# Kernel optimization log

Hardware: AMD Instinct MI355X
Metric: run time of the kernel (lower is better)

Reference implementation:

```python
import jax, jax.numpy as jnp
import numpy as np

B, S, HID = 1, 1024, 4096
NH, NKV, HD = 32, 8, 128
GROUPS = NH // NKV
THETA = 10000.0
SPAR = 0.5          # sparse_aggression (layer_idx > 0)
MIN_IDX = 4         # min_sparse_index: always-kept sink tokens
NEG = jnp.float32(-1e30)


def setup_inputs() -> dict:
    key = jax.random.key(0)
    k0, k1, k2, k3, k4 = jax.random.split(key, 5)
    sc = 0.02
    return {
        "hidden_states": jax.random.normal(k0, (B, S, HID), jnp.float32),
        "position_ids": jnp.arange(S, dtype=jnp.int32)[None, :],
        "Wq": jax.random.normal(k1, (NH * HD, HID), jnp.float32) * sc,
        "Wk": jax.random.normal(k2, (NKV * HD, HID), jnp.float32) * sc,
        "Wv": jax.random.normal(k3, (NKV * HD, HID), jnp.float32) * sc,
        "Wo": jax.random.normal(k4, (HID, NH * HD), jnp.float32) * sc,
    }


def _rotate_half(x):
    h = x.shape[-1] // 2
    return jnp.concatenate([-x[..., h:], x[..., :h]], axis=-1)


def _rope_cos_sin(position_ids):
    inv_freq = 1.0 / (THETA ** (jnp.arange(0, HD, 2, dtype=jnp.float32) / HD))
    freqs = position_ids.astype(jnp.float32)[..., None] * inv_freq  # [B,S,HD/2]
    emb = jnp.concatenate([freqs, freqs], axis=-1)                  # [B,S,HD]
    return jnp.cos(emb)[:, None], jnp.sin(emb)[:, None]             # [B,1,S,HD]


def reference(hidden_states, position_ids, Wq, Wk, Wv, Wo):
    b, s, _ = hidden_states.shape
    # QKV projections (nn.Linear: x @ W.T)
    q = (hidden_states @ Wq.T).reshape(b, s, NH, HD).transpose(0, 2, 1, 3)
    k = (hidden_states @ Wk.T).reshape(b, s, NKV, HD).transpose(0, 2, 1, 3)
    v = (hidden_states @ Wv.T).reshape(b, s, NKV, HD).transpose(0, 2, 1, 3)
    # RoPE
    cos, sin = _rope_cos_sin(position_ids)
    q = q * cos + _rotate_half(q) * sin
    k = k * cos + _rotate_half(k) * sin
    # repeat_kv (GQA expansion)
    k = jnp.repeat(k, GROUPS, axis=1)
    v = jnp.repeat(v, GROUPS, axis=1)
    # causal additive mask [1,1,S,S]
    causal = jnp.where(jnp.triu(jnp.ones((s, s), bool), 1), NEG, jnp.float32(0))[None, None]
    scale = 1.0 / np.sqrt(HD)
    scores = jnp.einsum('bhqd,bhkd->bhqk', q, k) * scale
    # oracle importance: softmax of (softmaxed) masked attention (no_grad in original)
    oracle = jax.nn.softmax((scores + causal).astype(jnp.float32), axis=-1)
    importance = jax.nn.softmax(oracle, axis=-1)
    importance = jax.lax.stop_gradient(importance)
    # descending sort -> rank of each key for each query
    sorted_idx = jnp.argsort(-importance, axis=-1)          # [B,H,S,S]
    ranks = jnp.argsort(sorted_idx, axis=-1)                # inverse perm
    # per-query token budget: keep ceil-ish top-k proportional to row length
    k_per_row = jnp.maximum((SPAR * (jnp.arange(s) + 1)).astype(jnp.int32), 1)
    key_idx = jnp.arange(s)
    kept = (ranks < k_per_row[None, None, :, None]) | (key_idx[None, None, None, :] < MIN_IDX)
    sparse_mask = jnp.where(kept, jnp.float32(0), NEG)
    # sparse attention
    attn = scores + sparse_mask + causal
    probs = jax.nn.softmax(attn.astype(jnp.float32), axis=-1).astype(v.dtype)
    out = jnp.einsum('bhqk,bhkd->bhqd', probs, v)           # [B,H,S,HD]
    out = out.transpose(0, 2, 1, 3).reshape(b, s, NH * HD)
    return out @ Wo.T
```

## Files before the change

kernel.cpp:

```cpp
#include <hip/hip_runtime.h>
#include <hip/hip_bf16.h>

#define S_LEN 1024
#define HID   4096
#define NH    32
#define NKV   8
#define HD    128
#define MIN_IDX 4
#define AO_COLS 4096
#define HEAD_STRIDE 131072

typedef __attribute__((ext_vector_type(8))) short short8;
typedef __attribute__((ext_vector_type(4))) float f32x4;

__device__ __forceinline__ unsigned short f2bf(float f) {
  union { float f; unsigned u; } v; v.f = f;
  unsigned r = v.u + 0x7FFFu + ((v.u >> 16) & 1u);
  return (unsigned short)(r >> 16);
}
__device__ __forceinline__ float bf2f(unsigned short h) {
  union { unsigned u; float f; } v; v.u = ((unsigned)h) << 16;
  return v.f;
}
__device__ __forceinline__ unsigned pk2(float a, float b) {
  union { __hip_bfloat162 h; unsigned u; } c;
  c.h = __float22bfloat162_rn(make_float2(a, b));
  return c.u;
}
__device__ __forceinline__ short8 pack8(float4 a, float4 b) {
  union { short8 s; unsigned u[4]; } r;
  r.u[0] = pk2(a.x, a.y); r.u[1] = pk2(a.z, a.w);
  r.u[2] = pk2(b.x, b.y); r.u[3] = pk2(b.z, b.w);
  return r.s;
}
__device__ __forceinline__ unsigned ordf(float f) {
  union { float f; int i; } v; v.f = f;
  return (unsigned)(v.i ^ ((v.i >> 31) | 0x80000000));
}
__device__ __forceinline__ float iordf(unsigned u) {
  union { int i; float f; } v;
  v.i = (u & 0x80000000u) ? (int)(u ^ 0x80000000u) : (int)~u;
  return v.f;
}
__device__ __forceinline__ float wave_sum_f(float v) {
  #pragma unroll
  for (int m = 32; m >= 1; m >>= 1) v += __shfl_xor(v, m);
  return v;
}
__device__ __forceinline__ unsigned wave_max_u(unsigned v) {
  #pragma unroll
  for (int m = 32; m >= 1; m >>= 1) { unsigned o = __shfl_xor(v, m); v = o > v ? o : v; }
  return v;
}
__device__ __forceinline__ void wave_lds_fence() {
  __builtin_amdgcn_s_waitcnt(0);
  __builtin_amdgcn_wave_barrier();
}
__device__ __forceinline__ void gload_lds16(const unsigned short* g, unsigned short* l) {
  auto gp = (const __attribute__((address_space(1))) unsigned*)g;
  auto lp = (__attribute__((address_space(3))) unsigned*)(unsigned)(unsigned long long)l;
  __builtin_amdgcn_global_load_lds(gp, lp, 16, 0, 0);
}

__global__ __launch_bounds__(256) void cvt_k(
    const float* __restrict__ src, unsigned short* __restrict__ dst)
{
  const size_t i = ((size_t)blockIdx.x * 256 + threadIdx.x) * 8;
  float4 a = *(const float4*)(src + i);
  float4 b = *(const float4*)(src + i + 4);
  *(short8*)(dst + i) = pack8(a, b);
}

__global__ __launch_bounds__(256) void gemm_qkv_k(
    const unsigned short* __restrict__ Xb, const unsigned short* __restrict__ Wb,
    unsigned short* __restrict__ Qraw, unsigned short* __restrict__ Kraw,
    unsigned short* __restrict__ Vt)
{
  __shared__ unsigned short As[128 * 32];
  __shared__ unsigned short Bs[128 * 32];
  const int nt = blockIdx.x;
  const int n0 = nt * 128;
  const int m0 = blockIdx.y * 128;
  const int t = threadIdx.x, w = t >> 6, lane = t & 63;
  const int wm = w >> 1, wn = w & 1;
  const int mcol = lane & 15, quad = lane >> 4;
  const int lrow = lane >> 2, lcol = (lane & 3) * 8;

  const unsigned short* Ag = Xb + (size_t)m0 * HID;
  const unsigned short* Bg = Wb + (size_t)n0 * HID;

  f32x4 acc[4][4];
  #pragma unroll
  for (int i = 0; i < 4; i++)
    #pragma unroll
    for (int j = 0; j < 4; j++) acc[i][j] = (f32x4){0.f, 0.f, 0.f, 0.f};

  for (int k0 = 0; k0 < HID; k0 += 32) {
    #pragma unroll
    for (int c2 = 0; c2 < 2; c2++) {
      const int c = w * 2 + c2;
      gload_lds16(Ag + (size_t)(c*16 + lrow) * HID + k0 + lcol, &As[c * 512]);
      gload_lds16(Bg + (size_t)(c*16 + lrow) * HID + k0 + lcol, &Bs[c * 512]);
    }
    __syncthreads();
    short8 af[4], bf[4];
    #pragma unroll
    for (int i = 0; i < 4; i++) af[i] = *(const short8*)&As[(wm*64 + i*16 + mcol)*32 + quad*8];
    #pragma unroll
    for (int j = 0; j < 4; j++) bf[j] = *(const short8*)&Bs[(wn*64 + j*16 + mcol)*32 + quad*8];
    #pragma unroll
    for (int i = 0; i < 4; i++)
      #pragma unroll
      for (int j = 0; j < 4; j++)
        acc[i][j] = __builtin_amdgcn_mfma_f32_16x16x32_bf16(af[i], bf[j], acc[i][j], 0, 0, 0);
    __syncthreads();
  }

  if (nt < 40) {
    unsigned short* dst = (nt < 32) ? (Qraw + (size_t)nt * HEAD_STRIDE)
                                    : (Kraw + (size_t)(nt - 32) * HEAD_STRIDE);
    #pragma unroll
    for (int i = 0; i < 4; i++) {
      const int rb = m0 + wm*64 + i*16 + quad*4;
      #pragma unroll
      for (int j = 0; j < 4; j++) {
        const int d = wn*64 + j*16 + mcol;
        #pragma unroll
        for (int r = 0; r < 4; r++)
          dst[(size_t)(rb + r) * HD + d] = f2bf(acc[i][j][r]);
      }
    }
  } else {
    unsigned short* dst = Vt + (size_t)(nt - 40) * HEAD_STRIDE;
    #pragma unroll
    for (int i = 0; i < 4; i++) {
      const int rb = m0 + wm*64 + i*16 + quad*4;
      #pragma unroll
      for (int j = 0; j < 4; j++) {
        const int d = wn*64 + j*16 + mcol;
        ushort4 v4;
        v4.x = f2bf(acc[i][j][0]); v4.y = f2bf(acc[i][j][1]);
        v4.z = f2bf(acc[i][j][2]); v4.w = f2bf(acc[i][j][3]);
        *(ushort4*)(dst + (size_t)d * S_LEN + rb) = v4;
      }
    }
  }
}

__global__ __launch_bounds__(256) void rope_qk_k(
    const int* __restrict__ pos_ids,
    unsigned short* __restrict__ Qraw, unsigned short* __restrict__ Kraw)
{
  const int w = threadIdx.x >> 6, lane = threadIdx.x & 63;
  const int gw = blockIdx.x * 4 + w;
  const int hidx = gw >> 10;
  const int s = gw & 1023;
  const float pos = (float)pos_ids[s];
  const float invf = powf(10000.0f, -(float)lane * (1.0f / 64.0f));
  float sn, cs;
  sincosf(pos * invf, &sn, &cs);
  unsigned short* base = (hidx < NH)
      ? (Qraw + (size_t)hidx * HEAD_STRIDE + (size_t)s * HD)
      : (Kraw + (size_t)(hidx - NH) * HEAD_STRIDE + (size_t)s * HD);
  const float x0 = bf2f(base[lane]), x1 = bf2f(base[lane + 64]);
  base[lane]      = f2bf(x0 * cs - x1 * sn);
  base[lane + 64] = f2bf(x1 * cs + x0 * sn);
}

#define PSTR 1040
template<int KT>
__device__ __forceinline__ void attn_body(
    const unsigned short* __restrict__ Qb, const unsigned short* __restrict__ Kh,
    const unsigned short* __restrict__ Vh, unsigned short* __restrict__ AO,
    unsigned short (*Pl)[PSTR], int (*hist)[256], float* rowinv,
    int q0, int h, int w, int lane, int mcol, int quad)
{
  constexpr int NC = 2 * KT;
  const float scale = 0.08838834764831845f;
  float (*scb)[16][130] = (float (*)[16][130])&Pl[0][0];

  short8 aq[4];
  {
    const unsigned short* qrow = Qb + ((size_t)h * S_LEN + q0 + mcol) * HD + quad * 8;
    #pragma unroll
    for (int kk = 0; kk < 4; kk++) aq[kk] = *(const short8*)(qrow + kk * 32);
  }

  unsigned su[4][NC];

  #pragma unroll
  for (int kt = 0; kt < KT; kt++) {
    short8 bfr[2][4];
    #pragma unroll
    for (int g2 = 0; g2 < 2; g2++) {
      const int key = kt * 128 + (w * 2 + g2) * 16 + mcol;
      const unsigned short* krow = Kh + (size_t)key * HD + quad * 8;
      #pragma unroll
      for (int kk = 0; kk < 4; kk++) bfr[g2][kk] = *(const short8*)(krow + kk * 32);
    }
    f32x4 d4[2];
    d4[0] = (f32x4){0.f,0.f,0.f,0.f}; d4[1] = (f32x4){0.f,0.f,0.f,0.f};
    #pragma unroll
    for (int g2 = 0; g2 < 2; g2++)
      #pragma unroll
      for (int kk = 0; kk < 4; kk++)
        d4[g2] = __builtin_amdgcn_mfma_f32_16x16x32_bf16(aq[kk], bfr[g2][kk], d4[g2], 0, 0, 0);
    #pragma unroll
    for (int g2 = 0; g2 < 2; g2++) {
      const int colc = (w * 2 + g2) * 16 + mcol;
      #pragma unroll
      for (int r = 0; r < 4; r++) scb[kt & 1][quad*4 + r][colc] = d4[g2][r] * scale;
    }
    __syncthreads();
    #pragma unroll
    for (int i = 0; i < 4; i++)
      #pragma unroll
      for (int sub = 0; sub < 2; sub++)
        su[i][kt*2 + sub] = ordf(scb[kt & 1][w*4 + i][sub*64 + lane]);
  }
  __syncthreads();

  #pragma unroll
  for (int i = 0; i < 4; i++) {
    const int r = w * 4 + i;
    const int q = q0 + r;
    const int L = q + 1;
    int ksel = L >> 1; if (ksel < 1) ksel = 1;

    unsigned prefix = 0, msk = 0;
    int krem = ksel;
    #pragma unroll
    for (int shift = 24; shift >= 0; shift -= 8) {
      { int4 z = {0, 0, 0, 0}; *(int4*)&hist[w][lane * 4] = z; }
      wave_lds_fence();
      #pragma unroll
      for (int c = 0; c < NC; c++) {
        const int j = c * 64 + lane;
        if (j < L && (su[i][c] & msk) == prefix)
          atomicAdd(&hist[w][(su[i][c] >> shift) & 255], 1);
      }
      wave_lds_fence();
      const int4 cv = *(const int4*)&hist[w][252 - lane * 4];
      int c4[4] = { cv.w, cv.z, cv.y, cv.x };
      const int lsum = c4[0] + c4[1] + c4[2] + c4[3];
      int x = lsum;
      #pragma unroll
      for (int d2 = 1; d2 < 64; d2 <<= 1) { int y = __shfl_up(x, d2); if (lane >= d2) x += y; }
      int run = x - lsum;
      int fbin = -1, fbefore = 0;
      #pragma unroll
      for (int j2 = 0; j2 < 4; j2++) {
        if (fbin < 0 && run < krem && run + c4[j2] >= krem) { fbin = 255 - lane*4 - j2; fbefore = run; }
        run += c4[j2];
      }
      unsigned long long bal = __ballot(fbin >= 0);
      int bin = 0, before = 0;
      if (bal != 0ull) {
        const int srcl = __ffsll((unsigned long long)bal) - 1;
        bin = __shfl(fbin, srcl);
        before = __shfl(fbefore, srcl);
        if (bin < 0) bin = 0;
      }
      krem -= before; if (krem < 1) krem = 1;
      prefix |= ((unsigned)bin) << shift;
      msk |= 0xFFu << shift;
    }
    const unsigned tau = prefix;
    const int tie_budget = krem;

    unsigned um = 0;
    #pragma unroll
    for (int c = 0; c < NC; c++) {
      const int j = c * 64 + lane;
      if (j < L && su[i][c] > um) um = su[i][c];
    }
    const float mx = iordf(wave_max_u(um));

    float ssum = 0.f;
    int tiebase = 0;
    #pragma unroll
    for (int c = 0; c < NC; c++) {
      const int j = c * 64 + lane;
      const bool act = j < L;
      const unsigned u = su[i][c];
      const bool eq = act && (u == tau);
      const unsigned long long bal = __ballot(eq);
      const int trank = tiebase + (int)__popcll(bal & ((1ull << lane) - 1ull));
      tiebase += (int)__popcll(bal);
      const bool kept = act && ((u > tau) || (eq && trank < tie_budget) || (j < MIN_IDX));
      const float e = kept ? __expf(iordf(u) - mx) : 0.f;
      Pl[r][c*64 + lane] = f2bf(e);
      ssum += e;
    }
    ssum = wave_sum_f(ssum);
    if (lane == 0) rowinv[r] = 1.f / fmaxf(ssum, 1e-30f);
  }
  __syncthreads();

  f32x4 opv[2];
  opv[0] = (f32x4){0.f,0.f,0.f,0.f}; opv[1] = (f32x4){0.f,0.f,0.f,0.f};
  #pragma unroll
  for (int kt = 0; kt < KT; kt++) {
    #pragma unroll
    for (int kb = 0; kb < 4; kb++) {
      short8 af = *(const short8*)&Pl[mcol][kt*128 + kb*32 + quad*8];
      #pragma unroll
      for (int n2 = 0; n2 < 2; n2++) {
        const int d = (w*2 + n2) * 16 + mcol;
        short8 bfr = *(const short8*)(Vh + (size_t)d * S_LEN + kt*128 + kb*32 + quad*8);
        opv[n2] = __builtin_amdgcn_mfma_f32_16x16x32_bf16(af, bfr, opv[n2], 0, 0, 0);
      }
    }
  }
  #pragma unroll
  for (int n2 = 0; n2 < 2; n2++) {
    const int col = h * HD + (w*2 + n2) * 16 + mcol;
    #pragma unroll
    for (int r2 = 0; r2 < 4; r2++) {
      const int row = q0 + quad*4 + r2;
      AO[(size_t)row * AO_COLS + col] = f2bf(opv[n2][r2] * rowinv[quad*4 + r2]);
    }
  }
}

__global__ __launch_bounds__(256, 4) void attn_k(
    const unsigned short* __restrict__ Qb, const unsigned short* __restrict__ Kb,
    const unsigned short* __restrict__ Vt, unsigned short* __restrict__ AO)
{
  __shared__ unsigned short Pl[16][PSTR];
  __shared__ int hist[4][256];
  __shared__ float rowinv[16];
  const int rb = (int)gridDim.x - 1 - (int)blockIdx.x;
  const int h = blockIdx.y;
  const int kvh = h >> 2;
  const int q0 = rb * 16;
  const int kt_max = (rb >> 3) + 1;
  const int t = threadIdx.x, w = t >> 6, lane = t & 63;
  const int mcol = lane & 15, quad = lane >> 4;
  const unsigned short* Kh = Kb + (size_t)kvh * HEAD_STRIDE;
  const unsigned short* Vh = Vt + (size_t)kvh * HEAD_STRIDE;

  switch (kt_max) {
    case 1: attn_body<1>(Qb, Kh, Vh, AO, Pl, hist, rowinv, q0, h, w, lane, mcol, quad); break;
    case 2: attn_body<2>(Qb, Kh, Vh, AO, Pl, hist, rowinv, q0, h, w, lane, mcol, quad); break;
    case 3: attn_body<3>(Qb, Kh, Vh, AO, Pl, hist, rowinv, q0, h, w, lane, mcol, quad); break;
    case 4: attn_body<4>(Qb, Kh, Vh, AO, Pl, hist, rowinv, q0, h, w, lane, mcol, quad); break;
    case 5: attn_body<5>(Qb, Kh, Vh, AO, Pl, hist, rowinv, q0, h, w, lane, mcol, quad); break;
    case 6: attn_body<6>(Qb, Kh, Vh, AO, Pl, hist, rowinv, q0, h, w, lane, mcol, quad); break;
    case 7: attn_body<7>(Qb, Kh, Vh, AO, Pl, hist, rowinv, q0, h, w, lane, mcol, quad); break;
    default: attn_body<8>(Qb, Kh, Vh, AO, Pl, hist, rowinv, q0, h, w, lane, mcol, quad); break;
  }
}

__global__ __launch_bounds__(256) void gemm_out_k(
    const unsigned short* __restrict__ A, const unsigned short* __restrict__ Wob,
    float* __restrict__ Out)
{
  __shared__ unsigned short As[128 * 32];
  __shared__ unsigned short Bs[128 * 32];
  const int n0 = blockIdx.x * 128;
  const int m0 = blockIdx.y * 128;
  const int t = threadIdx.x, w = t >> 6, lane = t & 63;
  const int wm = w >> 1, wn = w & 1;
  const int mcol = lane & 15, quad = lane >> 4;
  const int lrow = lane >> 2, lcol = (lane & 3) * 8;

  const unsigned short* Ag = A   + (size_t)m0 * AO_COLS;
  const unsigned short* Bg = Wob + (size_t)n0 * AO_COLS;

  f32x4 acc[4][4];
  #pragma unroll
  for (int i = 0; i < 4; i++)
    #pragma unroll
    for (int j = 0; j < 4; j++) acc[i][j] = (f32x4){0.f, 0.f, 0.f, 0.f};

  for (int k0 = 0; k0 < AO_COLS; k0 += 32) {
    #pragma unroll
    for (int c2 = 0; c2 < 2; c2++) {
      const int c = w * 2 + c2;
      gload_lds16(Ag + (size_t)(c*16 + lrow) * AO_COLS + k0 + lcol, &As[c * 512]);
      gload_lds16(Bg + (size_t)(c*16 + lrow) * AO_COLS + k0 + lcol, &Bs[c * 512]);
    }
    __syncthreads();
    short8 af[4], bf[4];
    #pragma unroll
    for (int i = 0; i < 4; i++) af[i] = *(const short8*)&As[(wm*64 + i*16 + mcol)*32 + quad*8];
    #pragma unroll
    for (int j = 0; j < 4; j++) bf[j] = *(const short8*)&Bs[(wn*64 + j*16 + mcol)*32 + quad*8];
    #pragma unroll
    for (int i = 0; i < 4; i++)
      #pragma unroll
      for (int j = 0; j < 4; j++)
        acc[i][j] = __builtin_amdgcn_mfma_f32_16x16x32_bf16(af[i], bf[j], acc[i][j], 0, 0, 0);
    __syncthreads();
  }
  #pragma unroll
  for (int i = 0; i < 4; i++) {
    const int rb = m0 + wm*64 + i*16 + quad*4;
    #pragma unroll
    for (int j = 0; j < 4; j++) {
      const int col = n0 + wn*64 + j*16 + mcol;
      #pragma unroll
      for (int r = 0; r < 4; r++)
        Out[(size_t)(rb + r) * HID + col] = acc[i][j][r];
    }
  }
}

extern "C" void kernel_launch(void* const* d_in, const int* in_sizes, int n_in,
                              void* d_out, int out_size, void* d_ws, size_t ws_size,
                              hipStream_t stream) {
  (void)in_sizes; (void)n_in; (void)out_size; (void)ws_size;
  const float* X   = (const float*)d_in[0];
  const int*   pos = (const int*)d_in[1];
  const float* Wq  = (const float*)d_in[2];
  const float* Wk  = (const float*)d_in[3];
  const float* Wv  = (const float*)d_in[4];
  const float* Wo  = (const float*)d_in[5];
  float* out = (float*)d_out;

  char* ws = (char*)d_ws;
  unsigned short* Qraw  = (unsigned short*)ws;
  unsigned short* Kraw  = (unsigned short*)(ws + 8388608);
  unsigned short* Vt    = (unsigned short*)(ws + 10485760);
  unsigned short* AO    = (unsigned short*)(ws + 12582912);
  unsigned short* Xb    = (unsigned short*)(ws + 20971520);
  unsigned short* Wqkvb = (unsigned short*)(ws + 29360128);
  unsigned short* Wob   = Wqkvb;

  cvt_k<<<dim3(2048), dim3(256), 0, stream>>>(X,  Xb);
  cvt_k<<<dim3(8192), dim3(256), 0, stream>>>(Wq, Wqkvb);
  cvt_k<<<dim3(2048), dim3(256), 0, stream>>>(Wk, Wqkvb + 16777216);
  cvt_k<<<dim3(2048), dim3(256), 0, stream>>>(Wv, Wqkvb + 20971520);

  gemm_qkv_k<<<dim3(48, 8),  dim3(256), 0, stream>>>(Xb, Wqkvb, Qraw, Kraw, Vt);
  rope_qk_k <<<dim3(10240),  dim3(256), 0, stream>>>(pos, Qraw, Kraw);

  cvt_k<<<dim3(8192), dim3(256), 0, stream>>>(Wo, Wob);

  attn_k    <<<dim3(64, 32), dim3(256), 0, stream>>>(Qraw, Kraw, Vt, AO);
  gemm_out_k<<<dim3(32, 8),  dim3(256), 0, stream>>>(AO, Wob, out);
}
```

Measured before the change: 546.5 us.

## Replace LDS radix-histogram top-k selection with ballot-based bitwise radix select

Replaces the per-row 4-pass, 8-bit LDS histogram with atomics and prefix scans by a bit-by-bit radix select. The new path uses wave ballots and popcounts over per-chunk active masks and starts at the highest bit that differs across the row. This removes LDS atomics, fences and the histogram buffer, which frees shared memory and may allow higher occupancy. In exchange it can take up to 32 serial iterations, each with 2·NC ballots, and the early exit depends on the data.

```diff
diff --git a/kernel.cpp b/kernel.cpp
--- a/kernel.cpp
+++ b/kernel.cpp
@@ -52,9 +52,15 @@
   for (int m = 32; m >= 1; m >>= 1) { unsigned o = __shfl_xor(v, m); v = o > v ? o : v; }
   return v;
 }
-__device__ __forceinline__ void wave_lds_fence() {
-  __builtin_amdgcn_s_waitcnt(0);
-  __builtin_amdgcn_wave_barrier();
+__device__ __forceinline__ unsigned wave_and_u(unsigned v) {
+  #pragma unroll
+  for (int m = 32; m >= 1; m >>= 1) v &= __shfl_xor(v, m);
+  return v;
+}
+__device__ __forceinline__ unsigned wave_or_u(unsigned v) {
+  #pragma unroll
+  for (int m = 32; m >= 1; m >>= 1) v |= __shfl_xor(v, m);
+  return v;
 }
 __device__ __forceinline__ void gload_lds16(const unsigned short* g, unsigned short* l) {
   auto gp = (const __attribute__((address_space(1))) unsigned*)g;
@@ -172,7 +178,7 @@
 __device__ __forceinline__ void attn_body(
     const unsigned short* __restrict__ Qb, const unsigned short* __restrict__ Kh,
     const unsigned short* __restrict__ Vh, unsigned short* __restrict__ AO,
-    unsigned short (*Pl)[PSTR], int (*hist)[256], float* rowinv,
+    unsigned short (*Pl)[PSTR], float* rowinv,
     int q0, int h, int w, int lane, int mcol, int quad)
 {
   constexpr int NC = 2 * KT;
@@ -220,6 +226,7 @@
   }
   __syncthreads();
 
+  const unsigned long long lmlt = (1ull << lane) - 1ull;
   #pragma unroll
   for (int i = 0; i < 4; i++) {
     const int r = w * 4 + i;
@@ -227,67 +234,63 @@
     const int L = q + 1;
     int ksel = L >> 1; if (ksel < 1) ksel = 1;
 
-    unsigned prefix = 0, msk = 0;
-    int krem = ksel;
-    #pragma unroll
-    for (int shift = 24; shift >= 0; shift -= 8) {
-      { int4 z = {0, 0, 0, 0}; *(int4*)&hist[w][lane * 4] = z; }
-      wave_lds_fence();
-      #pragma unroll
-      for (int c = 0; c < NC; c++) {
-        const int j = c * 64 + lane;
-        if (j < L && (su[i][c] & msk) == prefix)
-          atomicAdd(&hist[w][(su[i][c] >> shift) & 255], 1);
-      }
-      wave_lds_fence();
-      const int4 cv = *(const int4*)&hist[w][252 - lane * 4];
-      int c4[4] = { cv.w, cv.z, cv.y, cv.x };
-      const int lsum = c4[0] + c4[1] + c4[2] + c4[3];
-      int x = lsum;
-      #pragma unroll
-      for (int d2 = 1; d2 < 64; d2 <<= 1) { int y = __shfl_up(x, d2); if (lane >= d2) x += y; }
-      int run = x - lsum;
-      int fbin = -1, fbefore = 0;
-      #pragma unroll
-      for (int j2 = 0; j2 < 4; j2++) {
-        if (fbin < 0 && run < krem && run + c4[j2] >= krem) { fbin = 255 - lane*4 - j2; fbefore = run; }
-        run += c4[j2];
-      }
-      unsigned long long bal = __ballot(fbin >= 0);
-      int bin = 0, before = 0;
-      if (bal != 0ull) {
-        const int srcl = __ffsll((unsigned long long)bal) - 1;
-        bin = __shfl(fbin, srcl);
-        before = __shfl(fbefore, srcl);
-        if (bin < 0) bin = 0;
-      }
-      krem -= before; if (krem < 1) krem = 1;
-      prefix |= ((unsigned)bin) << shift;
-      msk |= 0xFFu << shift;
-    }
-    const unsigned tau = prefix;
-    const int tie_budget = krem;
-
-    unsigned um = 0;
+    unsigned long long M[NC];
+    #pragma unroll
+    for (int c = 0; c < NC; c++) {
+      const int rem = L - c * 64;
+      M[c] = rem >= 64 ? ~0ull : (rem <= 0 ? 0ull : ((1ull << rem) - 1ull));
+    }
+
+    unsigned um = 0, av = ~0u, ov = 0u;
     #pragma unroll
     for (int c = 0; c < NC; c++) {
       const int j = c * 64 + lane;
-      if (j < L && su[i][c] > um) um = su[i][c];
+      if (j < L) {
+        const unsigned u = su[i][c];
+        if (u > um) um = u;
+        av &= u; ov |= u;
+      }
     }
     const float mx = iordf(wave_max_u(um));
+    av = wave_and_u(av); ov = wave_or_u(ov);
+    const unsigned diff = av ^ ov;
+    const int hb = 31 - __builtin_clz(diff | 1u);
+    const unsigned highmask = (hb >= 31) ? 0u : ~((1u << (hb + 1)) - 1u);
+
+    int krem = ksel;
+    int tot = L;
+    unsigned tau = av & highmask, msk = highmask;
+    #pragma unroll 1
+    for (int b = hb; b >= 0; --b) {
+      if (tot <= krem) break;
+      const unsigned bitm = 1u << b;
+      int cnt = 0;
+      #pragma unroll
+      for (int c = 0; c < NC; c++)
+        if (M[c]) cnt += (int)__popcll(__ballot(su[i][c] & bitm) & M[c]);
+      const bool hi = cnt >= krem;
+      msk |= bitm;
+      if (hi) { tau |= bitm; tot = cnt; }
+      else    { krem -= cnt; tot -= cnt; }
+      #pragma unroll
+      for (int c = 0; c < NC; c++)
+        if (M[c]) {
+          const unsigned long long B = __ballot(su[i][c] & bitm);
+          M[c] &= hi ? B : ~B;
+        }
+    }
 
     float ssum = 0.f;
-    int tiebase = 0;
+    int cb = 0;
     #pragma unroll
     for (int c = 0; c < NC; c++) {
       const int j = c * 64 + lane;
-      const bool act = j < L;
       const unsigned u = su[i][c];
-      const bool eq = act && (u == tau);
-      const unsigned long long bal = __ballot(eq);
-      const int trank = tiebase + (int)__popcll(bal & ((1ull << lane) - 1ull));
-      tiebase += (int)__popcll(bal);
-      const bool kept = act && ((u > tau) || (eq && trank < tie_budget) || (j < MIN_IDX));
+      const unsigned umv = u & msk;
+      const int trank = cb + (int)__popcll(M[c] & lmlt);
+      cb += (int)__popcll(M[c]);
+      const bool kept = (j < L) &&
+          ((umv > tau) || (umv == tau && trank < krem) || (j < MIN_IDX));
       const float e = kept ? __expf(iordf(u) - mx) : 0.f;
       Pl[r][c*64 + lane] = f2bf(e);
       ssum += e;
@@ -328,7 +331,6 @@
     const unsigned short* __restrict__ Vt, unsigned short* __restrict__ AO)
 {
   __shared__ unsigned short Pl[16][PSTR];
-  __shared__ int hist[4][256];
   __shared__ float rowinv[16];
   const int rb = (int)gridDim.x - 1 - (int)blockIdx.x;
   const int h = blockIdx.y;
@@ -341,14 +343,14 @@
   const unsigned short* Vh = Vt + (size_t)kvh * HEAD_STRIDE;
 
   switch (kt_max) {
-    case 1: attn_body<1>(Qb, Kh, Vh, AO, Pl, hist, rowinv, q0, h, w, lane, mcol, quad); break;
-    case 2: attn_body<2>(Qb, Kh, Vh, AO, Pl, hist, rowinv, q0, h, w, lane, mcol, quad); break;
-    case 3: attn_body<3>(Qb, Kh, Vh, AO, Pl, hist, rowinv, q0, h, w, lane, mcol, quad); break;
-    case 4: attn_body<4>(Qb, Kh, Vh, AO, Pl, hist, rowinv, q0, h, w, lane, mcol, quad); break;
-    case 5: attn_body<5>(Qb, Kh, Vh, AO, Pl, hist, rowinv, q0, h, w, lane, mcol, quad); break;
-    case 6: attn_body<6>(Qb, Kh, Vh, AO, Pl, hist, rowinv, q0, h, w, lane, mcol, quad); break;
-    case 7: attn_body<7>(Qb, Kh, Vh, AO, Pl, hist, rowinv, q0, h, w, lane, mcol, quad); break;
-    default: attn_body<8>(Qb, Kh, Vh, AO, Pl, hist, rowinv, q0, h, w, lane, mcol, quad); break;
+    case 1: attn_body<1>(Qb, Kh, Vh, AO, Pl, rowinv, q0, h, w, lane, mcol, quad); break;
+    case 2: attn_body<2>(Qb, Kh, Vh, AO, Pl, rowinv, q0, h, w, lane, mcol, quad); break;
+    case 3: attn_body<3>(Qb, Kh, Vh, AO, Pl, rowinv, q0, h, w, lane, mcol, quad); break;
+    case 4: attn_body<4>(Qb, Kh, Vh, AO, Pl, rowinv, q0, h, w, lane, mcol, quad); break;
+    case 5: attn_body<5>(Qb, Kh, Vh, AO, Pl, rowinv, q0, h, w, lane, mcol, quad); break;
+    case 6: attn_body<6>(Qb, Kh, Vh, AO, Pl, rowinv, q0, h, w, lane, mcol, quad); break;
+    case 7: attn_body<7>(Qb, Kh, Vh, AO, Pl, rowinv, q0, h, w, lane, mcol, quad); break;
+    default: attn_body<8>(Qb, Kh, Vh, AO, Pl, rowinv, q0, h, w, lane, mcol, quad); break;
   }
 }
 
```

Result: slower. 603.4 us (+10.4%).

## Batch two rows per radix histogram pass and finish top-k with ballot bisection

Applied to the files above, without the earlier changes.

Restructures the per-row top-k threshold search in the attention kernel. Two rows now share one LDS histogram using 16-bit packed counts, and only the top two radix bytes go through histograms. The low 16 bits are resolved by a ballot/popcount bit-bisection that exits early once the remaining candidates fit the budget. The wave LDS fence now waits only on LDS counters instead of all counters. This removes half the histogram passes and their atomics, but adds a per-bit ballot loop over all chunks for rows with many ties.

```diff
diff --git a/kernel.cpp b/kernel.cpp
--- a/kernel.cpp
+++ b/kernel.cpp
@@ -53,7 +53,7 @@
   return v;
 }
 __device__ __forceinline__ void wave_lds_fence() {
-  __builtin_amdgcn_s_waitcnt(0);
+  __builtin_amdgcn_s_waitcnt(0xC07F);
   __builtin_amdgcn_wave_barrier();
 }
 __device__ __forceinline__ void gload_lds16(const unsigned short* g, unsigned short* l) {
@@ -172,7 +172,7 @@
 __device__ __forceinline__ void attn_body(
     const unsigned short* __restrict__ Qb, const unsigned short* __restrict__ Kh,
     const unsigned short* __restrict__ Vh, unsigned short* __restrict__ AO,
-    unsigned short (*Pl)[PSTR], int (*hist)[256], float* rowinv,
+    unsigned short (*Pl)[PSTR], unsigned (*hist)[256], float* rowinv,
     int q0, int h, int w, int lane, int mcol, int quad)
 {
   constexpr int NC = 2 * KT;
@@ -220,53 +220,97 @@
   }
   __syncthreads();
 
+  const unsigned long long lmlt = (1ull << lane) - 1ull;
+  int Lr[4], krem[4], tot[4];
+  unsigned prefix[4];
+  #pragma unroll
+  for (int i = 0; i < 4; i++) {
+    Lr[i] = q0 + w*4 + i + 1;
+    int ks = Lr[i] >> 1; if (ks < 1) ks = 1;
+    krem[i] = ks; tot[i] = Lr[i]; prefix[i] = 0u;
+  }
+
+  unsigned msk = 0u;
+  #pragma unroll
+  for (int pass = 0; pass < 2; pass++) {
+    const int shift = 24 - pass * 8;
+    #pragma unroll
+    for (int p = 0; p < 2; p++) {
+      { uint4 z = {0u, 0u, 0u, 0u}; *(uint4*)&hist[w][lane * 4] = z; }
+      wave_lds_fence();
+      #pragma unroll
+      for (int c = 0; c < NC; c++) {
+        const int j = c * 64 + lane;
+        #pragma unroll
+        for (int rr = 0; rr < 2; rr++) {
+          const int i = p * 2 + rr;
+          if (j < Lr[i] && (su[i][c] & msk) == prefix[i])
+            atomicAdd(&hist[w][(su[i][c] >> shift) & 255], 1u << (16 * rr));
+        }
+      }
+      wave_lds_fence();
+      const uint4 cv = *(const uint4*)&hist[w][252 - lane * 4];
+      unsigned c4[4] = { cv.w, cv.z, cv.y, cv.x };
+      const unsigned lsum = c4[0] + c4[1] + c4[2] + c4[3];
+      unsigned x = lsum;
+      #pragma unroll
+      for (int d2 = 1; d2 < 64; d2 <<= 1) { unsigned y = __shfl_up(x, d2); if (lane >= d2) x += y; }
+      const unsigned runp = x - lsum;
+      #pragma unroll
+      for (int rr = 0; rr < 2; rr++) {
+        const int i = p * 2 + rr;
+        const int sh16 = 16 * rr;
+        int run = (int)((runp >> sh16) & 0xFFFFu);
+        int fbin = -1, fbefore = 0, fcnt = 0;
+        #pragma unroll
+        for (int j2 = 0; j2 < 4; j2++) {
+          const int cnum = (int)((c4[j2] >> sh16) & 0xFFFFu);
+          if (fbin < 0 && run < krem[i] && run + cnum >= krem[i]) {
+            fbin = 255 - lane*4 - j2; fbefore = run; fcnt = cnum;
+          }
+          run += cnum;
+        }
+        const unsigned long long bal = __ballot(fbin >= 0);
+        int bin = 0, before = 0, cnt = krem[i];
+        if (bal != 0ull) {
+          const int srcl = __ffsll((unsigned long long)bal) - 1;
+          bin = __shfl(fbin, srcl);
+          before = __shfl(fbefore, srcl);
+          cnt = __shfl(fcnt, srcl);
+          if (bin < 0) bin = 0;
+        }
+        krem[i] -= before; if (krem[i] < 1) krem[i] = 1;
+        tot[i] = cnt;
+        prefix[i] |= ((unsigned)bin) << shift;
+      }
+    }
+    msk |= 0xFFu << (24 - pass * 8);
+  }
+
   #pragma unroll
   for (int i = 0; i < 4; i++) {
     const int r = w * 4 + i;
-    const int q = q0 + r;
-    const int L = q + 1;
-    int ksel = L >> 1; if (ksel < 1) ksel = 1;
-
-    unsigned prefix = 0, msk = 0;
-    int krem = ksel;
-    #pragma unroll
-    for (int shift = 24; shift >= 0; shift -= 8) {
-      { int4 z = {0, 0, 0, 0}; *(int4*)&hist[w][lane * 4] = z; }
-      wave_lds_fence();
+    const int L = Lr[i];
+    unsigned btau = prefix[i];
+    unsigned bmsk = 0xFFFF0000u;
+    int kr = krem[i];
+    int tt = tot[i];
+    #pragma unroll 1
+    for (int b = 15; b >= 0; --b) {
+      if (tt <= kr) break;
+      const unsigned bit = 1u << b;
+      const unsigned am = bmsk | bit;
+      const unsigned test = btau | bit;
+      int cnt = 0;
       #pragma unroll
       for (int c = 0; c < NC; c++) {
         const int j = c * 64 + lane;
-        if (j < L && (su[i][c] & msk) == prefix)
-          atomicAdd(&hist[w][(su[i][c] >> shift) & 255], 1);
-      }
-      wave_lds_fence();
-      const int4 cv = *(const int4*)&hist[w][252 - lane * 4];
-      int c4[4] = { cv.w, cv.z, cv.y, cv.x };
-      const int lsum = c4[0] + c4[1] + c4[2] + c4[3];
-      int x = lsum;
-      #pragma unroll
-      for (int d2 = 1; d2 < 64; d2 <<= 1) { int y = __shfl_up(x, d2); if (lane >= d2) x += y; }
-      int run = x - lsum;
-      int fbin = -1, fbefore = 0;
-      #pragma unroll
-      for (int j2 = 0; j2 < 4; j2++) {
-        if (fbin < 0 && run < krem && run + c4[j2] >= krem) { fbin = 255 - lane*4 - j2; fbefore = run; }
-        run += c4[j2];
-      }
-      unsigned long long bal = __ballot(fbin >= 0);
-      int bin = 0, before = 0;
-      if (bal != 0ull) {
-        const int srcl = __ffsll((unsigned long long)bal) - 1;
-        bin = __shfl(fbin, srcl);
-        before = __shfl(fbefore, srcl);
-        if (bin < 0) bin = 0;
-      }
-      krem -= before; if (krem < 1) krem = 1;
-      prefix |= ((unsigned)bin) << shift;
-      msk |= 0xFFu << shift;
-    }
-    const unsigned tau = prefix;
-    const int tie_budget = krem;
+        cnt += (int)__popcll(__ballot(j < L && (su[i][c] & am) == test));
+      }
+      if (cnt >= kr) { btau = test; tt = cnt; }
+      else           { kr -= cnt; tt -= cnt; }
+      bmsk = am;
+    }
 
     unsigned um = 0;
     #pragma unroll
@@ -281,13 +325,14 @@
     #pragma unroll
     for (int c = 0; c < NC; c++) {
       const int j = c * 64 + lane;
-      const bool act = j < L;
       const unsigned u = su[i][c];
-      const bool eq = act && (u == tau);
+      const unsigned umv = u & bmsk;
+      const bool eq = (j < L) && (umv == btau);
       const unsigned long long bal = __ballot(eq);
-      const int trank = tiebase + (int)__popcll(bal & ((1ull << lane) - 1ull));
+      const int trank = tiebase + (int)__popcll(bal & lmlt);
       tiebase += (int)__popcll(bal);
-      const bool kept = act && ((u > tau) || (eq && trank < tie_budget) || (j < MIN_IDX));
+      const bool kept = (j < L) &&
+          ((umv > btau) || (eq && trank < kr) || (j < MIN_IDX));
       const float e = kept ? __expf(iordf(u) - mx) : 0.f;
       Pl[r][c*64 + lane] = f2bf(e);
       ssum += e;
@@ -328,7 +373,7 @@
     const unsigned short* __restrict__ Vt, unsigned short* __restrict__ AO)
 {
   __shared__ unsigned short Pl[16][PSTR];
-  __shared__ int hist[4][256];
+  __shared__ unsigned hist[4][256];
   __shared__ float rowinv[16];
   const int rb = (int)gridDim.x - 1 - (int)blockIdx.x;
   const int h = blockIdx.y;
```

After: 537.2 us. No clear change (-1.7%).
